# Performance work log

Hardware: AMD Instinct MI355X
Metric: run time of the kernel (lower is better)

## Reference

```python
import jax, jax.numpy as jnp
import numpy as np

N, H, M, D = 128, 512, 2048, 128  # batch, dim_h_o, dim_C2_1, dim_C2_2
EPS = 1e-8
LN2 = float(np.log(2.0))


def _cos_sim(a, b, eps=EPS):
    # torch.nn.CosineSimilarity over last dim with eps clamp on norms
    num = jnp.sum(a * b, axis=-1)
    na = jnp.maximum(jnp.sqrt(jnp.sum(a * a, axis=-1)), eps)
    nb = jnp.maximum(jnp.sqrt(jnp.sum(b * b, axis=-1)), eps)
    return num / (na * nb)


def setup_inputs() -> dict:
    key = jax.random.key(0)
    ks = jax.random.split(key, 16)
    s = 0.02
    return {
        "h_o_prev": jax.random.normal(ks[0], (N, H), jnp.float32),
        "c_prev": jax.random.normal(ks[1], (N, M, D), jnp.float32),
        "c_xf": jax.random.normal(ks[2], (N, M, D), jnp.float32),
        "Wk": jax.random.normal(ks[3], (D, H), jnp.float32) * s,
        "bk": jnp.zeros((D,), jnp.float32),
        "Wb": jax.random.normal(ks[4], (1, H), jnp.float32) * s,
        "bb": jnp.zeros((1,), jnp.float32),
        "We": jax.random.normal(ks[5], (D, H), jnp.float32) * s,
        "be": jnp.zeros((D,), jnp.float32),
        "Wv": jax.random.normal(ks[6], (D, H), jnp.float32) * s,
        "bv": jnp.zeros((D,), jnp.float32),
        "W_ih": jax.random.normal(ks[7], (3 * H, D), jnp.float32) * s,
        "W_hh": jax.random.normal(ks[8], (3 * H, H), jnp.float32) * s,
        "b_ih": jnp.zeros((3 * H,), jnp.float32),
        "b_hh": jnp.zeros((3 * H,), jnp.float32),
    }


def _gru_cell(x, h, W_ih, W_hh, b_ih, b_hh):
    # torch GRUCell: gates ordered (reset, update, new)
    gi = x @ W_ih.T + b_ih
    gh = h @ W_hh.T + b_hh
    i_r, i_z, i_n = jnp.split(gi, 3, axis=-1)
    h_r, h_z, h_n = jnp.split(gh, 3, axis=-1)
    r = jax.nn.sigmoid(i_r + h_r)
    z = jax.nn.sigmoid(i_z + h_z)
    n = jnp.tanh(i_n + r * h_n)
    return (1.0 - z) * n + z * h


def reference(h_o_prev, c_prev, c_xf, Wk, bk, Wb, bb, We, be, Wv, bv, W_ih, W_hh, b_ih, b_hh):
    # key / key-strength
    k = h_o_prev @ Wk.T + bk                       # [N, D]
    beta_pre = h_o_prev @ Wb.T + bb                # [N, 1]
    beta_pos = jnp.maximum(beta_pre, 0.0)
    beta_neg = jnp.minimum(beta_pre, 0.0)
    beta = (jnp.log1p(jnp.exp(beta_neg)) + beta_pos
            + jnp.log1p(jnp.exp(-beta_pos)) + (1.0 - LN2))  # softplus(x)+1

    # read addressing over c_xf
    s_kx = _cos_sim(c_xf, k[:, None, :])           # [N, M]
    w_kx = jax.nn.softmax(s_kx * beta, axis=1)     # [N, M]
    r = jnp.einsum('nm,nmd->nd', w_kx, c_xf)       # [N, D]

    # write addressing over c_prev
    s_kc = _cos_sim(c_prev, k[:, None, :])         # [N, M]
    w_kc = jax.nn.softmax(s_kc * beta, axis=1)     # [N, M]

    # controller update
    h_o = _gru_cell(r, h_o_prev, W_ih, W_hh, b_ih, b_hh)  # [N, H]

    # erase / add memory write
    e = jax.nn.sigmoid(h_o @ We.T + be)            # [N, D]
    v = h_o @ Wv.T + bv                            # [N, D]
    w2 = w_kc[:, :, None]                          # [N, M, 1]
    c_new = c_prev * (1.0 - w2 * e[:, None, :]) + w2 * v[:, None, :]
    return (h_o, c_new)
```

## Files before the change

### kernel.cpp

```cpp
#include <hip/hip_runtime.h>
#include <math.h>

#define NN 128
#define HH 512
#define MM 2048
#define DD 128
#define EPSF 1e-8f


typedef float vfloat4 __attribute__((ext_vector_type(4)));

__device__ inline float4 ntload4(const float4* p) {
    vfloat4 r = __builtin_nontemporal_load((const vfloat4*)p);
    return make_float4(r.x, r.y, r.z, r.w);
}
__device__ inline void ntstore4(float4* p, float4 v) {
    vfloat4 r = {v.x, v.y, v.z, v.w};
    __builtin_nontemporal_store(r, (vfloat4*)p);
}

__global__ void k1a_kgemm(const float* __restrict__ h, const float* __restrict__ Wk,
                          const float* __restrict__ bk, float* __restrict__ k) {
    int bI = blockIdx.x;
    int jt = bI & 7, nt = bI >> 3;
    int t  = threadIdx.x;
    int tn = t & 15, tj = t >> 4;
    __shared__ float act[16][132];
    __shared__ float wt[16][132];
    int lbase = t * 8;
    int lrow  = lbase >> 7, lcol = lbase & 127;
    float acc = 0.f;
    for (int c = 0; c < 4; ++c) {
        int koff = c * 128;
        const float4* s = (const float4*)(h + (nt * 16 + lrow) * HH + koff + lcol);
        *(float4*)&act[lrow][lcol]     = s[0];
        *(float4*)&act[lrow][lcol + 4] = s[1];
        const float4* w = (const float4*)(Wk + (jt * 16 + lrow) * HH + koff + lcol);
        *(float4*)&wt[lrow][lcol]      = w[0];
        *(float4*)&wt[lrow][lcol + 4]  = w[1];
        __syncthreads();
        const float* ar = act[tn];
        const float* wr = wt[tj];
        #pragma unroll
        for (int kk = 0; kk < 128; kk += 4) {
            float4 a4 = *(const float4*)(ar + kk);
            float4 w4 = *(const float4*)(wr + kk);
            acc += a4.x * w4.x + a4.y * w4.y + a4.z * w4.z + a4.w * w4.w;
        }
        __syncthreads();
    }
    k[(nt * 16 + tn) * DD + jt * 16 + tj] = acc + bk[jt * 16 + tj];
}

__global__ void k1b_knbeta(const float* __restrict__ h, const float* __restrict__ kq,
                           const float* __restrict__ Wb, const float* __restrict__ bb,
                           float* __restrict__ kn, float* __restrict__ beta) {
    int n = blockIdx.x;
    int t = threadIdx.x;
    __shared__ float red[128];
    float kk = kq[n * DD + t];
    red[t] = kk * kk;
    __syncthreads();
    for (int s = 64; s > 0; s >>= 1) { if (t < s) red[t] += red[t + s]; __syncthreads(); }
    if (t == 0) kn[n] = fmaxf(sqrtf(red[0]), EPSF);
    __syncthreads();
    float b = 0.f;
    for (int i = t; i < HH; i += 128) b += h[n * HH + i] * Wb[i];
    red[t] = b;
    __syncthreads();
    for (int s = 64; s > 0; s >>= 1) { if (t < s) red[t] += red[t + s]; __syncthreads(); }
    if (t == 0) {
        float bp   = red[0] + bb[0];
        float bpos = fmaxf(bp, 0.f);
        float bneg = fminf(bp, 0.f);
        beta[n] = log1pf(expf(bneg)) + bpos + log1pf(expf(-bpos))
                + (1.f - 0.69314718055994530942f);
    }
}

__global__ void kX_xf(const float* __restrict__ c_xf, const float* __restrict__ kv,
                      const float* __restrict__ kn, const float* __restrict__ beta,
                      float* __restrict__ rp, float* __restrict__ clx) {
    int b = blockIdx.x;
    int chunk = b & 31, n = b >> 5;
    int t = threadIdx.x;
    int q = t & 7, rr = t >> 3;
    __shared__ float wsum[4];
    __shared__ float4 part[32][33];
    const float4* k4p = (const float4*)(kv + n * DD);
    float4 kq[4];
    #pragma unroll
    for (int j = 0; j < 4; j++) kq[j] = k4p[j * 8 + q];
    const float4* src4 = (const float4*)c_xf + (size_t)(n * MM + chunk * 64) * 32;
    float4 x0[4], x1[4];
    #pragma unroll
    for (int j = 0; j < 4; j++) {
        x0[j] = ntload4(src4 + rr * 32 + j * 8 + q);
        x1[j] = ntload4(src4 + (rr + 32) * 32 + j * 8 + q);
    }
    float dk0 = 0.f, nn0 = 0.f, dk1 = 0.f, nn1 = 0.f;
    #pragma unroll
    for (int j = 0; j < 4; j++) {
        dk0 += x0[j].x * kq[j].x + x0[j].y * kq[j].y + x0[j].z * kq[j].z + x0[j].w * kq[j].w;
        nn0 += x0[j].x * x0[j].x + x0[j].y * x0[j].y + x0[j].z * x0[j].z + x0[j].w * x0[j].w;
        dk1 += x1[j].x * kq[j].x + x1[j].y * kq[j].y + x1[j].z * kq[j].z + x1[j].w * kq[j].w;
        nn1 += x1[j].x * x1[j].x + x1[j].y * x1[j].y + x1[j].z * x1[j].z + x1[j].w * x1[j].w;
    }
    #pragma unroll
    for (int m = 1; m < 8; m <<= 1) {
        dk0 += __shfl_xor(dk0, m);
        nn0 += __shfl_xor(nn0, m);
        dk1 += __shfl_xor(dk1, m);
        nn1 += __shfl_xor(nn1, m);
    }
    float sb = beta[n] / kn[n];
    float p0 = expf(dk0 / fmaxf(sqrtf(nn0), EPSF) * sb);
    float p1 = expf(dk1 / fmaxf(sqrtf(nn1), EPSF) * sb);
    float ls = p0 + p1;
    #pragma unroll
    for (int m = 8; m < 64; m <<= 1) ls += __shfl_xor(ls, m);
    if ((t & 63) == 0) wsum[t >> 6] = ls;
    float4 acc[4];
    #pragma unroll
    for (int j = 0; j < 4; j++) {
        acc[j].x = p0 * x0[j].x + p1 * x1[j].x;
        acc[j].y = p0 * x0[j].y + p1 * x1[j].y;
        acc[j].z = p0 * x0[j].z + p1 * x1[j].z;
        acc[j].w = p0 * x0[j].w + p1 * x1[j].w;
    }
    #pragma unroll
    for (int j = 0; j < 4; j++) part[rr][j * 8 + q] = acc[j];
    __syncthreads();
    if (t == 0) clx[n * 32 + chunk] = wsum[0] + wsum[1] + wsum[2] + wsum[3];
    if (t < 128) {
        int qd = t >> 2, c2 = t & 3;
        float4 s = part[c2 * 8][qd];
        #pragma unroll
        for (int i = 1; i < 8; i++) {
            float4 pp = part[c2 * 8 + i][qd];
            s.x += pp.x; s.y += pp.y; s.z += pp.z; s.w += pp.w;
        }
        #pragma unroll
        for (int m = 1; m < 4; m <<= 1) {
            s.x += __shfl_xor(s.x, m);
            s.y += __shfl_xor(s.y, m);
            s.z += __shfl_xor(s.z, m);
            s.w += __shfl_xor(s.w, m);
        }
        if (c2 == 0) ((float4*)rp)[(size_t)(n * 32 + chunk) * 32 + qd] = s;
    }
}

__global__ void kP_prev(const float* __restrict__ c_prev, const float* __restrict__ kv,
                        const float* __restrict__ kn, const float* __restrict__ beta,
                        float* __restrict__ sc, float* __restrict__ clc) {
    int b = blockIdx.x;
    int chunk = b & 31, n = b >> 5;
    int t = threadIdx.x;
    int q = t & 7, rr = t >> 3;
    __shared__ float wsum[4];
    const float4* k4p = (const float4*)(kv + n * DD);
    float4 kq[4];
    #pragma unroll
    for (int j = 0; j < 4; j++) kq[j] = k4p[j * 8 + q];
    const float4* src4 = (const float4*)c_prev + (size_t)(n * MM + chunk * 64) * 32;
    float dk0 = 0.f, nn0 = 0.f, dk1 = 0.f, nn1 = 0.f;
    #pragma unroll
    for (int j = 0; j < 4; j++) {
        float4 a = src4[rr * 32 + j * 8 + q];
        float4 c = src4[(rr + 32) * 32 + j * 8 + q];
        dk0 += a.x * kq[j].x + a.y * kq[j].y + a.z * kq[j].z + a.w * kq[j].w;
        nn0 += a.x * a.x + a.y * a.y + a.z * a.z + a.w * a.w;
        dk1 += c.x * kq[j].x + c.y * kq[j].y + c.z * kq[j].z + c.w * kq[j].w;
        nn1 += c.x * c.x + c.y * c.y + c.z * c.z + c.w * c.w;
    }
    #pragma unroll
    for (int m = 1; m < 8; m <<= 1) {
        dk0 += __shfl_xor(dk0, m);
        nn0 += __shfl_xor(nn0, m);
        dk1 += __shfl_xor(dk1, m);
        nn1 += __shfl_xor(nn1, m);
    }
    float sb = beta[n] / kn[n];
    float p0 = expf(dk0 / fmaxf(sqrtf(nn0), EPSF) * sb);
    float p1 = expf(dk1 / fmaxf(sqrtf(nn1), EPSF) * sb);
    if (q == 0) {
        sc[n * MM + chunk * 64 + rr] = p0;
        sc[n * MM + chunk * 64 + rr + 32] = p1;
    }
    float ls = p0 + p1;
    #pragma unroll
    for (int m = 8; m < 64; m <<= 1) ls += __shfl_xor(ls, m);
    if ((t & 63) == 0) wsum[t >> 6] = ls;
    __syncthreads();
    if (t == 0) clc[n * 32 + chunk] = wsum[0] + wsum[1] + wsum[2] + wsum[3];
}

__global__ void kB1_r(const float* __restrict__ rp, const float* __restrict__ clx,
                      float* __restrict__ r) {
    int n = blockIdx.x;
    int t = threadIdx.x;
    float L = 0.f, acc = 0.f;
    for (int c = 0; c < 32; c++) {
        L   += clx[n * 32 + c];
        acc += rp[((size_t)n * 32 + c) * 128 + t];
    }
    r[n * DD + t] = acc / L;
}

__global__ void kB2_invL(const float* __restrict__ clc, float* __restrict__ invLc) {
    int n = threadIdx.x;
    float L = 0.f;
    for (int c = 0; c < 32; c++) L += clc[n * 32 + c];
    invLc[n] = 1.f / L;
}

__global__ void g1_gemm(const float* __restrict__ rf, const float* __restrict__ h,
                        const float* __restrict__ Wih, const float* __restrict__ Whh,
                        const float* __restrict__ bih, const float* __restrict__ bhh,
                        float* __restrict__ A, float* __restrict__ B) {
    int bI = blockIdx.x;
    int jt = bI % 96, nt = bI / 96;
    int t  = threadIdx.x;
    int tn = t & 15, tj = t >> 4;
    int n  = nt * 16 + tn;
    int j  = jt * 16 + tj;
    __shared__ float act[16][132];
    __shared__ float wt[16][132];
    int lbase = t * 8;
    int lrow  = lbase >> 7, lcol = lbase & 127;
    float accA = 0.f, accB = 0.f;
    for (int c = 0; c < 5; ++c) {
        if (c == 0) {
            int gn = nt * 16 + lrow;
            const float4* s = (const float4*)(rf + gn * DD + lcol);
            *(float4*)&act[lrow][lcol]     = s[0];
            *(float4*)&act[lrow][lcol + 4] = s[1];
            const float4* w = (const float4*)(Wih + (jt * 16 + lrow) * DD + lcol);
            *(float4*)&wt[lrow][lcol]      = w[0];
            *(float4*)&wt[lrow][lcol + 4]  = w[1];
        } else {
            int koff = (c - 1) * 128;
            const float4* s = (const float4*)(h + (nt * 16 + lrow) * HH + koff + lcol);
            *(float4*)&act[lrow][lcol]     = s[0];
            *(float4*)&act[lrow][lcol + 4] = s[1];
            const float4* w = (const float4*)(Whh + (jt * 16 + lrow) * HH + koff + lcol);
            *(float4*)&wt[lrow][lcol]      = w[0];
            *(float4*)&wt[lrow][lcol + 4]  = w[1];
        }
        __syncthreads();
        float acc = 0.f;
        const float* ar = act[tn];
        const float* wr = wt[tj];
        #pragma unroll
        for (int kk = 0; kk < 128; kk += 4) {
            float4 a4 = *(const float4*)(ar + kk);
            float4 w4 = *(const float4*)(wr + kk);
            acc += a4.x * w4.x + a4.y * w4.y + a4.z * w4.z + a4.w * w4.w;
        }
        if (c == 0) accA = acc; else accB += acc;
        __syncthreads();
    }
    A[n * 1536 + j] = accA + bih[j];
    B[n * 1536 + j] = accB + bhh[j];
}

__global__ void g2_gates(const float* __restrict__ A, const float* __restrict__ B,
                         const float* __restrict__ hprev, float* __restrict__ ho) {
    int id = blockIdx.x * 256 + threadIdx.x;
    int n = id >> 9, j = id & 511;
    const float* a = A + n * 1536;
    const float* b = B + n * 1536;
    float ir = a[j], iz = a[512 + j], in_ = a[1024 + j];
    float hr = b[j], hz = b[512 + j], hn  = b[1024 + j];
    float rg = 1.f / (1.f + expf(-(ir + hr)));
    float zg = 1.f / (1.f + expf(-(iz + hz)));
    float ng = tanhf(in_ + rg * hn);
    ho[id] = (1.f - zg) * ng + zg * hprev[id];
}

__global__ void g3_ev(const float* __restrict__ ho, const float* __restrict__ We,
                      const float* __restrict__ be, const float* __restrict__ Wv,
                      const float* __restrict__ bv, float* __restrict__ e,
                      float* __restrict__ v) {
    int bI = blockIdx.x;
    int jt = bI % 16, nt = bI / 16;
    int t  = threadIdx.x;
    int tn = t & 15, tj = t >> 4;
    int n  = nt * 16 + tn;
    int j  = jt * 16 + tj;
    __shared__ float act[16][132];
    __shared__ float wt[16][132];
    int lbase = t * 8;
    int lrow  = lbase >> 7, lcol = lbase & 127;
    int wrow  = jt * 16 + lrow;
    const float* Wsrc = (wrow < 128) ? (We + wrow * HH) : (Wv + (wrow - 128) * HH);
    float acc = 0.f;
    for (int c = 0; c < 4; ++c) {
        int koff = c * 128;
        const float4* s = (const float4*)(ho + (nt * 16 + lrow) * HH + koff + lcol);
        *(float4*)&act[lrow][lcol]     = s[0];
        *(float4*)&act[lrow][lcol + 4] = s[1];
        const float4* w = (const float4*)(Wsrc + koff + lcol);
        *(float4*)&wt[lrow][lcol]      = w[0];
        *(float4*)&wt[lrow][lcol + 4]  = w[1];
        __syncthreads();
        const float* ar = act[tn];
        const float* wr = wt[tj];
        #pragma unroll
        for (int kk = 0; kk < 128; kk += 4) {
            float4 a4 = *(const float4*)(ar + kk);
            float4 w4 = *(const float4*)(wr + kk);
            acc += a4.x * w4.x + a4.y * w4.y + a4.z * w4.z + a4.w * w4.w;
        }
        __syncthreads();
    }
    if (j < 128) e[n * DD + j] = 1.f / (1.f + expf(-(acc + be[j])));
    else         v[n * DD + (j - 128)] = acc + bv[j - 128];
}

__global__ void k6_cnew(const float* __restrict__ c_prev, const float* __restrict__ sc,
                        const float* __restrict__ invLc, const float* __restrict__ e,
                        const float* __restrict__ v, float* __restrict__ out) {
    int i  = blockIdx.x * 256 + threadIdx.x;
    int nm = i >> 5;
    int d4 = i & 31;
    int n  = nm >> 11;
    float w = sc[nm] * invLc[n];
    float4 c4 = ((const float4*)c_prev)[i];
    float4 e4 = ((const float4*)e)[n * 32 + d4];
    float4 v4 = ((const float4*)v)[n * 32 + d4];
    float4 o;
    o.x = c4.x * (1.f - w * e4.x) + w * v4.x;
    o.y = c4.y * (1.f - w * e4.y) + w * v4.y;
    o.z = c4.z * (1.f - w * e4.z) + w * v4.z;
    o.w = c4.w * (1.f - w * e4.w) + w * v4.w;
    ntstore4((float4*)out + i, o);
}

extern "C" void kernel_launch(void* const* d_in, const int* in_sizes, int n_in,
                              void* d_out, int out_size, void* d_ws, size_t ws_size,
                              hipStream_t stream) {
    const float* h_o_prev = (const float*)d_in[0];
    const float* c_prev   = (const float*)d_in[1];
    const float* c_xf     = (const float*)d_in[2];
    const float* Wk       = (const float*)d_in[3];
    const float* bk       = (const float*)d_in[4];
    const float* Wb       = (const float*)d_in[5];
    const float* bb       = (const float*)d_in[6];
    const float* We       = (const float*)d_in[7];
    const float* be       = (const float*)d_in[8];
    const float* Wv       = (const float*)d_in[9];
    const float* bv       = (const float*)d_in[10];
    const float* Wih      = (const float*)d_in[11];
    const float* Whh      = (const float*)d_in[12];
    const float* bih      = (const float*)d_in[13];
    const float* bhh      = (const float*)d_in[14];

    float* ws    = (float*)d_ws;
    float* k     = ws;
    float* kn    = ws + 16384;
    float* beta  = ws + 16512;
    float* sc    = ws + 16640;
    float* rp    = ws + 278784;
    float* clx   = ws + 807168;
    float* clc   = ws + 815360;
    float* r     = ws + 819456;
    float* invLc = ws + 835968;
    float* e     = ws + 836096;
    float* v     = ws + 852480;
    float* Ag    = ws + 278784;
    float* Bg    = ws + 475392;

    float* ho_out = (float*)d_out;
    float* c_out  = (float*)d_out + NN * HH;

    k1a_kgemm<<<64, 256, 0, stream>>>(h_o_prev, Wk, bk, k);
    k1b_knbeta<<<NN, 128, 0, stream>>>(h_o_prev, k, Wb, bb, kn, beta);
    kX_xf<<<NN * 32, 256, 0, stream>>>(c_xf, k, kn, beta, rp, clx);
    kB1_r<<<NN, 128, 0, stream>>>(rp, clx, r);
    g1_gemm<<<768, 256, 0, stream>>>(r, h_o_prev, Wih, Whh, bih, bhh, Ag, Bg);
    g2_gates<<<NN * HH / 256, 256, 0, stream>>>(Ag, Bg, h_o_prev, ho_out);
    g3_ev<<<128, 256, 0, stream>>>(ho_out, We, be, Wv, bv, e, v);
    kP_prev<<<NN * 32, 256, 0, stream>>>(c_prev, k, kn, beta, sc, clc);
    kB2_invL<<<1, 128, 0, stream>>>(clc, invLc);
    k6_cnew<<<NN * MM * DD / 4 / 256, 256, 0, stream>>>(c_prev, sc, invLc, e, v, c_out);
}
```

Baseline: 128.6 us.

## Merge reduction kernels, reorder c_prev scoring, batch more work per thread, use fast exp

Several independent changes land together. kP_prev now handles two 64-row chunks per block with all loads issued up front, and it is launched right after the c_xf pass instead of after the GRU. kB2_invL is folded into the r-reduction kernel, so there is one fewer launch. k6_cnew processes two float4 per thread. expf is replaced by __expf in several kernels. The aim is to cut launch overhead and improve memory-level parallelism, at a small accuracy cost from the fast exp and with possible cache-locality changes between c_prev passes.

```diff
diff --git a/kernel.cpp b/kernel.cpp
--- a/kernel.cpp
+++ b/kernel.cpp
@@ -114,8 +114,8 @@
         nn1 += __shfl_xor(nn1, m);
     }
     float sb = beta[n] / kn[n];
-    float p0 = expf(dk0 / fmaxf(sqrtf(nn0), EPSF) * sb);
-    float p1 = expf(dk1 / fmaxf(sqrtf(nn1), EPSF) * sb);
+    float p0 = __expf(dk0 / fmaxf(sqrtf(nn0), EPSF) * sb);
+    float p1 = __expf(dk1 / fmaxf(sqrtf(nn1), EPSF) * sb);
     float ls = p0 + p1;
     #pragma unroll
     for (int m = 8; m < 64; m <<= 1) ls += __shfl_xor(ls, m);
@@ -155,49 +155,74 @@
                         const float* __restrict__ kn, const float* __restrict__ beta,
                         float* __restrict__ sc, float* __restrict__ clc) {
     int b = blockIdx.x;
-    int chunk = b & 31, n = b >> 5;
+    int pair = b & 15, n = b >> 4;
+    int chunk0 = pair * 2, chunk1 = chunk0 + 1;
     int t = threadIdx.x;
     int q = t & 7, rr = t >> 3;
-    __shared__ float wsum[4];
+    __shared__ float wsumA[4], wsumB[4];
     const float4* k4p = (const float4*)(kv + n * DD);
     float4 kq[4];
     #pragma unroll
     for (int j = 0; j < 4; j++) kq[j] = k4p[j * 8 + q];
-    const float4* src4 = (const float4*)c_prev + (size_t)(n * MM + chunk * 64) * 32;
-    float dk0 = 0.f, nn0 = 0.f, dk1 = 0.f, nn1 = 0.f;
+    const float4* s0 = (const float4*)c_prev + (size_t)(n * MM + chunk0 * 64) * 32;
+    const float4* s1 = (const float4*)c_prev + (size_t)(n * MM + chunk1 * 64) * 32;
+    float4 a0[4], a1[4], b0[4], b1[4];
     #pragma unroll
     for (int j = 0; j < 4; j++) {
-        float4 a = src4[rr * 32 + j * 8 + q];
-        float4 c = src4[(rr + 32) * 32 + j * 8 + q];
-        dk0 += a.x * kq[j].x + a.y * kq[j].y + a.z * kq[j].z + a.w * kq[j].w;
-        nn0 += a.x * a.x + a.y * a.y + a.z * a.z + a.w * a.w;
-        dk1 += c.x * kq[j].x + c.y * kq[j].y + c.z * kq[j].z + c.w * kq[j].w;
-        nn1 += c.x * c.x + c.y * c.y + c.z * c.z + c.w * c.w;
+        a0[j] = s0[rr * 32 + j * 8 + q];
+        a1[j] = s0[(rr + 32) * 32 + j * 8 + q];
+        b0[j] = s1[rr * 32 + j * 8 + q];
+        b1[j] = s1[(rr + 32) * 32 + j * 8 + q];
+    }
+    float dA0 = 0.f, nA0 = 0.f, dA1 = 0.f, nA1 = 0.f;
+    float dB0 = 0.f, nB0 = 0.f, dB1 = 0.f, nB1 = 0.f;
+    #pragma unroll
+    for (int j = 0; j < 4; j++) {
+        dA0 += a0[j].x * kq[j].x + a0[j].y * kq[j].y + a0[j].z * kq[j].z + a0[j].w * kq[j].w;
+        nA0 += a0[j].x * a0[j].x + a0[j].y * a0[j].y + a0[j].z * a0[j].z + a0[j].w * a0[j].w;
+        dA1 += a1[j].x * kq[j].x + a1[j].y * kq[j].y + a1[j].z * kq[j].z + a1[j].w * kq[j].w;
+        nA1 += a1[j].x * a1[j].x + a1[j].y * a1[j].y + a1[j].z * a1[j].z + a1[j].w * a1[j].w;
+        dB0 += b0[j].x * kq[j].x + b0[j].y * kq[j].y + b0[j].z * kq[j].z + b0[j].w * kq[j].w;
+        nB0 += b0[j].x * b0[j].x + b0[j].y * b0[j].y + b0[j].z * b0[j].z + b0[j].w * b0[j].w;
+        dB1 += b1[j].x * kq[j].x + b1[j].y * kq[j].y + b1[j].z * kq[j].z + b1[j].w * kq[j].w;
+        nB1 += b1[j].x * b1[j].x + b1[j].y * b1[j].y + b1[j].z * b1[j].z + b1[j].w * b1[j].w;
     }
     #pragma unroll
     for (int m = 1; m < 8; m <<= 1) {
-        dk0 += __shfl_xor(dk0, m);
-        nn0 += __shfl_xor(nn0, m);
-        dk1 += __shfl_xor(dk1, m);
-        nn1 += __shfl_xor(nn1, m);
+        dA0 += __shfl_xor(dA0, m); nA0 += __shfl_xor(nA0, m);
+        dA1 += __shfl_xor(dA1, m); nA1 += __shfl_xor(nA1, m);
+        dB0 += __shfl_xor(dB0, m); nB0 += __shfl_xor(nB0, m);
+        dB1 += __shfl_xor(dB1, m); nB1 += __shfl_xor(nB1, m);
     }
     float sb = beta[n] / kn[n];
-    float p0 = expf(dk0 / fmaxf(sqrtf(nn0), EPSF) * sb);
-    float p1 = expf(dk1 / fmaxf(sqrtf(nn1), EPSF) * sb);
+    float pA0 = __expf(dA0 / fmaxf(sqrtf(nA0), EPSF) * sb);
+    float pA1 = __expf(dA1 / fmaxf(sqrtf(nA1), EPSF) * sb);
+    float pB0 = __expf(dB0 / fmaxf(sqrtf(nB0), EPSF) * sb);
+    float pB1 = __expf(dB1 / fmaxf(sqrtf(nB1), EPSF) * sb);
     if (q == 0) {
-        sc[n * MM + chunk * 64 + rr] = p0;
-        sc[n * MM + chunk * 64 + rr + 32] = p1;
-    }
-    float ls = p0 + p1;
-    #pragma unroll
-    for (int m = 8; m < 64; m <<= 1) ls += __shfl_xor(ls, m);
-    if ((t & 63) == 0) wsum[t >> 6] = ls;
+        float* srow = sc + n * MM;
+        srow[chunk0 * 64 + rr]      = pA0;
+        srow[chunk0 * 64 + rr + 32] = pA1;
+        srow[chunk1 * 64 + rr]      = pB0;
+        srow[chunk1 * 64 + rr + 32] = pB1;
+    }
+    float lsA = pA0 + pA1, lsB = pB0 + pB1;
+    #pragma unroll
+    for (int m = 8; m < 64; m <<= 1) {
+        lsA += __shfl_xor(lsA, m);
+        lsB += __shfl_xor(lsB, m);
+    }
+    if ((t & 63) == 0) { wsumA[t >> 6] = lsA; wsumB[t >> 6] = lsB; }
     __syncthreads();
-    if (t == 0) clc[n * 32 + chunk] = wsum[0] + wsum[1] + wsum[2] + wsum[3];
-}
-
-__global__ void kB1_r(const float* __restrict__ rp, const float* __restrict__ clx,
-                      float* __restrict__ r) {
+    if (t == 0) {
+        clc[n * 32 + chunk0] = wsumA[0] + wsumA[1] + wsumA[2] + wsumA[3];
+        clc[n * 32 + chunk1] = wsumB[0] + wsumB[1] + wsumB[2] + wsumB[3];
+    }
+}
+
+__global__ void kBall(const float* __restrict__ rp, const float* __restrict__ clx,
+                      const float* __restrict__ clc, float* __restrict__ r,
+                      float* __restrict__ invLc) {
     int n = blockIdx.x;
     int t = threadIdx.x;
     float L = 0.f, acc = 0.f;
@@ -206,13 +231,11 @@
         acc += rp[((size_t)n * 32 + c) * 128 + t];
     }
     r[n * DD + t] = acc / L;
-}
-
-__global__ void kB2_invL(const float* __restrict__ clc, float* __restrict__ invLc) {
-    int n = threadIdx.x;
-    float L = 0.f;
-    for (int c = 0; c < 32; c++) L += clc[n * 32 + c];
-    invLc[n] = 1.f / L;
+    if (n == 0) {
+        float L2 = 0.f;
+        for (int c = 0; c < 32; c++) L2 += clc[t * 32 + c];
+        invLc[t] = 1.f / L2;
+    }
 }
 
 __global__ void g1_gemm(const float* __restrict__ rf, const float* __restrict__ h,
@@ -273,8 +296,8 @@
     const float* b = B + n * 1536;
     float ir = a[j], iz = a[512 + j], in_ = a[1024 + j];
     float hr = b[j], hz = b[512 + j], hn  = b[1024 + j];
-    float rg = 1.f / (1.f + expf(-(ir + hr)));
-    float zg = 1.f / (1.f + expf(-(iz + hz)));
+    float rg = 1.f / (1.f + __expf(-(ir + hr)));
+    float zg = 1.f / (1.f + __expf(-(iz + hz)));
     float ng = tanhf(in_ + rg * hn);
     ho[id] = (1.f - zg) * ng + zg * hprev[id];
 }
@@ -315,27 +338,31 @@
         }
         __syncthreads();
     }
-    if (j < 128) e[n * DD + j] = 1.f / (1.f + expf(-(acc + be[j])));
+    if (j < 128) e[n * DD + j] = 1.f / (1.f + __expf(-(acc + be[j])));
     else         v[n * DD + (j - 128)] = acc + bv[j - 128];
 }
 
 __global__ void k6_cnew(const float* __restrict__ c_prev, const float* __restrict__ sc,
                         const float* __restrict__ invLc, const float* __restrict__ e,
                         const float* __restrict__ v, float* __restrict__ out) {
-    int i  = blockIdx.x * 256 + threadIdx.x;
-    int nm = i >> 5;
-    int d4 = i & 31;
-    int n  = nm >> 11;
-    float w = sc[nm] * invLc[n];
-    float4 c4 = ((const float4*)c_prev)[i];
-    float4 e4 = ((const float4*)e)[n * 32 + d4];
-    float4 v4 = ((const float4*)v)[n * 32 + d4];
-    float4 o;
-    o.x = c4.x * (1.f - w * e4.x) + w * v4.x;
-    o.y = c4.y * (1.f - w * e4.y) + w * v4.y;
-    o.z = c4.z * (1.f - w * e4.z) + w * v4.z;
-    o.w = c4.w * (1.f - w * e4.w) + w * v4.w;
-    ntstore4((float4*)out + i, o);
+    int base = blockIdx.x * 512 + threadIdx.x;
+    #pragma unroll
+    for (int u = 0; u < 2; u++) {
+        int i  = base + u * 256;
+        int nm = i >> 5;
+        int d4 = i & 31;
+        int n  = nm >> 11;
+        float w = sc[nm] * invLc[n];
+        float4 c4 = ((const float4*)c_prev)[i];
+        float4 e4 = ((const float4*)e)[n * 32 + d4];
+        float4 v4 = ((const float4*)v)[n * 32 + d4];
+        float4 o;
+        o.x = c4.x * (1.f - w * e4.x) + w * v4.x;
+        o.y = c4.y * (1.f - w * e4.y) + w * v4.y;
+        o.z = c4.z * (1.f - w * e4.z) + w * v4.z;
+        o.w = c4.w * (1.f - w * e4.w) + w * v4.w;
+        ntstore4((float4*)out + i, o);
+    }
 }
 
 extern "C" void kernel_launch(void* const* d_in, const int* in_sizes, int n_in,
@@ -378,11 +405,10 @@
     k1a_kgemm<<<64, 256, 0, stream>>>(h_o_prev, Wk, bk, k);
     k1b_knbeta<<<NN, 128, 0, stream>>>(h_o_prev, k, Wb, bb, kn, beta);
     kX_xf<<<NN * 32, 256, 0, stream>>>(c_xf, k, kn, beta, rp, clx);
-    kB1_r<<<NN, 128, 0, stream>>>(rp, clx, r);
+    kP_prev<<<NN * 16, 256, 0, stream>>>(c_prev, k, kn, beta, sc, clc);
+    kBall<<<NN, 128, 0, stream>>>(rp, clx, clc, r, invLc);
     g1_gemm<<<768, 256, 0, stream>>>(r, h_o_prev, Wih, Whh, bih, bhh, Ag, Bg);
     g2_gates<<<NN * HH / 256, 256, 0, stream>>>(Ag, Bg, h_o_prev, ho_out);
     g3_ev<<<128, 256, 0, stream>>>(ho_out, We, be, Wv, bv, e, v);
-    kP_prev<<<NN * 32, 256, 0, stream>>>(c_prev, k, kn, beta, sc, clc);
-    kB2_invL<<<1, 128, 0, stream>>>(clc, invLc);
-    k6_cnew<<<NN * MM * DD / 4 / 256, 256, 0, stream>>>(c_prev, sc, invLc, e, v, c_out);
-}
+    k6_cnew<<<NN * MM * DD / 8 / 256, 256, 0, stream>>>(c_prev, sc, invLc, e, v, c_out);
+}
```

Result: no change. 127.0 us (-1.2%).
